# Kernel optimization log

Measured on AMD Instinct MI355X. Metric: run time of the kernel, lower is better.

The kernel has to match this reference:

```python
import jax, jax.numpy as jnp
import numpy as np

PI = float(np.pi)          # ouro.pi_center
THIRD = 2.0 * PI / 3.0     # ouro.third_offset
EPB = PI                   # ouro.effective_pi_boundary
DEV = 0.01                 # ouro.deviation
SPARSITY = 0.75
NH = 8
EPS = 1e-5


def prune(w):
    # ouroboros_prune_revive: elementwise resonance chain + quantile threshold mask
    s = w.size
    bloom = jnp.clip(jnp.sin(w * PI), -1.0, 1.0)  # noise_level = 0 (deterministic)
    theta = jnp.linspace(0.0, float(s), s).reshape(w.shape)
    bloom = bloom + bloom * jnp.cos(theta / float(s) + THIRD) * 1.5  # rebound_amp
    etched = jnp.cos(bloom * (EPB ** 2)) + bloom * bloom * (DEV / PI)
    thr = jnp.quantile(jnp.abs(etched), 1.0 - SPARSITY)
    mask = (jnp.abs(etched) > thr).astype(w.dtype)
    return w * mask


def layernorm(x, g, b):
    m = jnp.mean(x, axis=-1, keepdims=True)
    v = jnp.var(x, axis=-1, keepdims=True)
    return (x - m) * jax.lax.rsqrt(v + EPS) * g + b


def setup_inputs():
    key = jax.random.key(0)
    V, D, L, F, B, S = 10000, 512, 6, 2048, 16, 512
    ks = jax.random.split(key, 9)
    p = lambda k, sh: jax.random.normal(k, sh, jnp.float32) * 0.02
    return dict(
        src=jax.random.randint(ks[0], (B, S), 0, V),
        emb=p(ks[1], (V, D)),
        pos=p(ks[2], (1, 512, D)),
        in_proj_w=p(ks[3], (L, 3 * D, D)), in_proj_b=jnp.zeros((L, 3 * D), jnp.float32),
        out_proj_w=p(ks[4], (L, D, D)), out_proj_b=jnp.zeros((L, D), jnp.float32),
        ln1_g=jnp.ones((L, D), jnp.float32), ln1_b=jnp.zeros((L, D), jnp.float32),
        ln2_g=jnp.ones((L, D), jnp.float32), ln2_b=jnp.zeros((L, D), jnp.float32),
        lin1_w=p(ks[5], (L, F, D)), lin1_b=jnp.zeros((L, F), jnp.float32),
        lin2_w=p(ks[6], (L, D, F)), lin2_b=jnp.zeros((L, D), jnp.float32),
        out_w=p(ks[7], (V, D)), out_b=jnp.zeros((V,), jnp.float32),
    )


def reference(src, emb, pos, in_proj_w, in_proj_b, out_proj_w, out_proj_b,
              ln1_g, ln1_b, ln2_g, ln2_b, lin1_w, lin1_b, lin2_w, lin2_b,
              out_w, out_b):
    B, S = src.shape
    D = emb.shape[1]
    L = in_proj_w.shape[0]
    H, dh = NH, D // NH
    x = emb[src] * jnp.sqrt(jnp.float32(D)) + pos[:, :S, :]
    for l in range(L):
        wi = prune(in_proj_w[l])
        qkv = x @ wi.T + in_proj_b[l]
        q, k, v = jnp.split(qkv, 3, axis=-1)
        q = q.reshape(B, S, H, dh)
        k = k.reshape(B, S, H, dh)
        v = v.reshape(B, S, H, dh)
        scores = jnp.einsum('bqhd,bkhd->bhqk', q, k) / jnp.sqrt(jnp.float32(dh))
        att = jax.nn.softmax(scores, axis=-1)
        o = jnp.einsum('bhqk,bkhd->bqhd', att, v).reshape(B, S, D)
        o = o @ out_proj_w[l].T + out_proj_b[l]
        x = layernorm(x + o, ln1_g[l], ln1_b[l])  # post-norm
        w1 = prune(lin1_w[l])
        w2 = prune(lin2_w[l])
        ff = jax.nn.relu(x @ w1.T + lin1_b[l]) @ w2.T + lin2_b[l]
        x = layernorm(x + ff, ln2_g[l], ln2_b[l])
    return x @ out_w.T + out_b
```

## Files before the change

kernel.cpp:

```cpp
#include <hip/hip_runtime.h>
#include <math.h>

#define MTOK   8192
#define DMODEL 512
#define DFF    2048
#define NLAYER 6
#define VOCAB  10000
#define VPAD   10112
#define NHEAD  8
#define DHEAD  64

typedef __attribute__((ext_vector_type(8))) __bf16 bf16x8;
typedef __attribute__((ext_vector_type(4))) float  f32x4;

static const size_t X_B     = 0;
static const size_t Y_B     = (size_t)MTOK * DMODEL * 4;
static const size_t SH_B    = Y_B * 2;
static const size_t WH_B    = SH_B + (size_t)MTOK * DFF * 4;
static const size_t WL_B    = WH_B + (size_t)DFF * DMODEL * 2;
static const size_t HIST_B  = WL_B + (size_t)DFF * DMODEL * 2;
static const size_t STATE_B = HIST_B + (size_t)36 * 4096 * 4;
static const size_t THR_B   = STATE_B + (size_t)36 * 32;
static const size_t WS_BASE = THR_B + 18 * 8;
static const size_t BITS_B  = (WS_BASE + 255) & ~(size_t)255;
static const size_t WS_BITS = BITS_B + (size_t)17301504 / 8;

struct PState {
    double lo, hi;
    unsigned int rank;
    unsigned int pad;
    unsigned long long found;
};

__device__ __forceinline__ unsigned short f2b(float f)
{
    unsigned int u = __float_as_uint(f);
    u += 0x7fffu + ((u >> 16) & 1u);
    return (unsigned short)(u >> 16);
}
__device__ __forceinline__ float b2f(unsigned short h)
{
    return __uint_as_float(((unsigned int)h) << 16);
}

__device__ __forceinline__ void gload16(const void* g, void* l)
{
    __builtin_amdgcn_global_load_lds(
        (const __attribute__((address_space(1))) unsigned int*)g,
        (__attribute__((address_space(3))) unsigned int*)l, 16, 0, 0);
}

__device__ __forceinline__ double etched_abs(float wv, int i, double step, double invn)
{
    float b0 = sinf(wv * 3.14159274f);
    b0 = fminf(1.0f, fmaxf(-1.0f, b0));
    double theta = step * (double)i;
    double c = cos(theta * invn + 2.0943951023931953);
    double bl = (double)b0;
    double bloom = bl + bl * c * 1.5;
    double e = cos(bloom * 9.869604401089358)
             + bloom * bloom * 0.003183098861837907;
    return fabs(e);
}

__device__ __forceinline__ void prune_matrix(int m, const float* ipw, const float* w1,
                                             const float* w2, const float** w, int* n)
{
    int l = m / 3, j = m % 3;
    if (j == 0)      { *w = ipw + (size_t)l * 786432;  *n = 786432;  }
    else if (j == 1) { *w = w1  + (size_t)l * 1048576; *n = 1048576; }
    else             { *w = w2  + (size_t)l * 1048576; *n = 1048576; }
}

__device__ __forceinline__ size_t moff9(int j)
{
    int c0 = (j + 2) / 3;
    return (size_t)c0 * 786432 + (size_t)(j - c0) * 1048576;
}
static __host__ __device__ inline size_t prune_soff(int m)
{
    int c0 = (m + 2) / 3;
    return (size_t)c0 * 786432 + (size_t)(m - c0) * 1048576;
}

__global__ __launch_bounds__(256) void k_prune_init(unsigned int* hist, PState* st)
{
    int gid = blockIdx.x * 256 + threadIdx.x;
    for (int i = gid; i < 36 * 4096; i += gridDim.x * 256) hist[i] = 0u;
    if (gid < 36) {
        int m = gid >> 1;
        int n = (m % 3 == 0) ? 786432 : 1048576;
        st[gid].lo = 0.0;
        st[gid].hi = 1.03;
        st[gid].rank = (unsigned)(n / 4 - 1 + (gid & 1));
        st[gid].found = 0x7FF0000000000000ULL;
    }
}

__global__ __launch_bounds__(256) void k_eval(const float* ipw, const float* w1,
                                              const float* w2, double* E, int mb0)
{
    int j = blockIdx.x >> 7;
    int chunk = blockIdx.x & 127;
    int m = mb0 + j;
    const float* w; int n;
    prune_matrix(m, ipw, w1, w2, &w, &n);
    double* Em = E + moff9(j);
    double step = (double)n / (double)(n - 1);
    double invn = 1.0 / (double)n;
    int per = (n + 127) >> 7;
    int i0 = chunk * per;
    int i1 = min(n, i0 + per);
    for (int i = i0 + (int)threadIdx.x; i < i1; i += 256)
        Em[i] = etched_abs(w[i], i, step, invn);
}

__global__ __launch_bounds__(256) void k_hist_E(const double* __restrict__ E,
                                                unsigned int* hist, PState* st, int mb0)
{
    int j = blockIdx.x >> 6;
    int chunk = blockIdx.x & 63;
    int m = mb0 + j;
    int n = (m % 3 == 0) ? 786432 : 1048576;
    const double* Em = E + moff9(j);
    __shared__ unsigned int h[2][4096];
    for (int i = threadIdx.x; i < 8192; i += 256) ((unsigned int*)h)[i] = 0u;
    __syncthreads();
    double lo0 = st[2*m].lo,   hi0 = st[2*m].hi;
    double lo1 = st[2*m+1].lo, hi1 = st[2*m+1].hi;
    double sc0 = 4096.0 / (hi0 - lo0);
    double sc1 = 4096.0 / (hi1 - lo1);
    int per = (n + 63) >> 6;
    int i0 = chunk * per;
    int i1 = min(n, i0 + per);
    for (int i = i0 + (int)threadIdx.x; i < i1; i += 256) {
        double a = Em[i];
        if (a >= lo0 && a < hi0) {
            int bin = (int)((a - lo0) * sc0); if (bin > 4095) bin = 4095;
            atomicAdd(&h[0][bin], 1u);
        }
        if (a >= lo1 && a < hi1) {
            int bin = (int)((a - lo1) * sc1); if (bin > 4095) bin = 4095;
            atomicAdd(&h[1][bin], 1u);
        }
    }
    __syncthreads();
    for (int i = threadIdx.x; i < 4096; i += 256) {
        if (h[0][i]) atomicAdd(&hist[(size_t)(2*m) * 4096 + i], h[0][i]);
        if (h[1][i]) atomicAdd(&hist[(size_t)(2*m+1) * 4096 + i], h[1][i]);
    }
}

__global__ __launch_bounds__(256) void k_prune_select(unsigned int* hist, PState* st,
                                                      int mb0)
{
    int s = mb0 * 2 + blockIdx.x;
    __shared__ unsigned int h[4096];
    unsigned int* gh = hist + (size_t)s * 4096;
    for (int i = threadIdx.x; i < 4096; i += 256) { h[i] = gh[i]; gh[i] = 0u; }
    __syncthreads();
    if (threadIdx.x == 0) {
        PState ps = st[s];
        unsigned int r = ps.rank;
        unsigned int acc = 0;
        int bsel = -1; unsigned int newr = 0;
        for (int bi = 0; bi < 4096; ++bi) {
            unsigned int c = h[bi];
            if (bsel < 0 && r < acc + c) { bsel = bi; newr = r - acc; }
            acc += c;
        }
        if (bsel < 0) {
            for (int bi = 4095; bi >= 0; --bi)
                if (h[bi]) { bsel = bi; newr = h[bi] - 1; break; }
            if (bsel < 0) { bsel = 0; newr = 0; }
        }
        double width = (ps.hi - ps.lo) / 4096.0;
        st[s].lo = ps.lo + width * bsel;
        st[s].hi = ps.lo + width * (bsel + 1);
        st[s].rank = newr;
    }
}

__global__ __launch_bounds__(256) void k_capture_E(const double* __restrict__ E,
                                                   PState* st, int mb0)
{
    int j = blockIdx.x >> 6;
    int chunk = blockIdx.x & 63;
    int m = mb0 + j;
    int n = (m % 3 == 0) ? 786432 : 1048576;
    const double* Em = E + moff9(j);
    double lo0 = st[2*m].lo, lo1 = st[2*m+1].lo;
    unsigned long long mn0 = 0x7FF0000000000000ULL, mn1 = 0x7FF0000000000000ULL;
    int per = (n + 63) >> 6;
    int i0 = chunk * per;
    int i1 = min(n, i0 + per);
    for (int i = i0 + (int)threadIdx.x; i < i1; i += 256) {
        double a = Em[i];
        unsigned long long bits = (unsigned long long)__double_as_longlong(a);
        if (a >= lo0 && bits < mn0) mn0 = bits;
        if (a >= lo1 && bits < mn1) mn1 = bits;
    }
    __shared__ unsigned long long sm[2];
    if (threadIdx.x == 0) { sm[0] = 0x7FF0000000000000ULL; sm[1] = 0x7FF0000000000000ULL; }
    __syncthreads();
    atomicMin(&sm[0], mn0);
    atomicMin(&sm[1], mn1);
    __syncthreads();
    if (threadIdx.x == 0) {
        atomicMin(&st[2*m].found, sm[0]);
        atomicMin(&st[2*m+1].found, sm[1]);
    }
}

__global__ void k_thr_batch(PState* st, double* thr, int mb0)
{
    int t = threadIdx.x;
    if (t < 9) {
        int m = mb0 + t;
        double v0 = __longlong_as_double((long long)st[2*m].found);
        double v1 = __longlong_as_double((long long)st[2*m+1].found);
        thr[m] = v0 + 0.75 * (v1 - v0);
    }
}

__global__ __launch_bounds__(256) void k_bits(const double* __restrict__ E,
                                              const double* __restrict__ thr,
                                              unsigned long long* __restrict__ bits,
                                              int mb0)
{
    int j = blockIdx.y;
    int m = mb0 + j;
    int n = (m % 3 == 0) ? 786432 : 1048576;
    double T = thr[m];
    const double* Em = E + moff9(j);
    unsigned long long* bm = bits + (prune_soff(m) >> 6);
    int nw = n >> 6;
    int lane = threadIdx.x & 63;
    int wid = (blockIdx.x * 256 + threadIdx.x) >> 6;
    int nwaves = gridDim.x * 4;
    for (int w = wid; w < nw; w += nwaves) {
        bool p = Em[(w << 6) + lane] > T;
        unsigned long long b = __ballot(p);
        if (lane == 0) bm[w] = b;
    }
}

__global__ __launch_bounds__(256) void k_mask_bits(const float* __restrict__ w,
                                                   unsigned short* __restrict__ oh,
                                                   unsigned short* __restrict__ ol,
                                                   const unsigned long long* __restrict__ bits,
                                                   int n)
{
    int stride = gridDim.x * 256 * 4;
    for (int i4 = (blockIdx.x * 256 + threadIdx.x) * 4; i4 < n; i4 += stride) {
        float4 v = *(const float4*)(w + i4);
        unsigned long long word = bits[i4 >> 6];
        int sh = i4 & 63;
        float x0 = (word >> (sh + 0)) & 1 ? v.x : 0.0f;
        float x1 = (word >> (sh + 1)) & 1 ? v.y : 0.0f;
        float x2 = (word >> (sh + 2)) & 1 ? v.z : 0.0f;
        float x3 = (word >> (sh + 3)) & 1 ? v.w : 0.0f;
        unsigned short h0 = f2b(x0), h1 = f2b(x1), h2 = f2b(x2), h3 = f2b(x3);
        uint2 hv, lv;
        hv.x = (unsigned)h0 | ((unsigned)h1 << 16);
        hv.y = (unsigned)h2 | ((unsigned)h3 << 16);
        lv.x = (unsigned)f2b(x0 - b2f(h0)) | ((unsigned)f2b(x1 - b2f(h1)) << 16);
        lv.y = (unsigned)f2b(x2 - b2f(h2)) | ((unsigned)f2b(x3 - b2f(h3)) << 16);
        *(uint2*)(oh + i4) = hv;
        *(uint2*)(ol + i4) = lv;
    }
}

__global__ __launch_bounds__(256) void k_apply_mask_split(const float* __restrict__ w,
                                                          unsigned short* __restrict__ oh,
                                                          unsigned short* __restrict__ ol,
                                                          const double* __restrict__ thr,
                                                          int m, int n)
{
    double T = thr[m];
    double step = (double)n / (double)(n - 1);
    double invn = 1.0 / (double)n;
    for (int i = blockIdx.x * 256 + threadIdx.x; i < n; i += gridDim.x * 256) {
        double a = etched_abs(w[i], i, step, invn);
        float v = (a > T) ? w[i] : 0.0f;
        unsigned short h = f2b(v);
        oh[i] = h;
        ol[i] = f2b(v - b2f(h));
    }
}

__global__ __launch_bounds__(256) void k_split(const float* __restrict__ w,
                                               unsigned short* __restrict__ oh,
                                               unsigned short* __restrict__ ol,
                                               int n, int total)
{
    for (int i = blockIdx.x * 256 + threadIdx.x; i < total; i += gridDim.x * 256) {
        float v = (i < n) ? w[i] : 0.0f;
        unsigned short h = f2b(v);
        oh[i] = h;
        ol[i] = f2b(v - b2f(h));
    }
}

__global__ __launch_bounds__(256) void k_embed(const int* __restrict__ src,
                                               const float* __restrict__ emb,
                                               const float* __restrict__ pos,
                                               float* __restrict__ x,
                                               unsigned short* __restrict__ xh,
                                               unsigned short* __restrict__ xl)
{
    int t = blockIdx.x;
    int tid = threadIdx.x;
    int v = src[t];
    int s = t & 511;
    const float* e = emb + (size_t)v * DMODEL;
    const float* p = pos + (size_t)s * DMODEL;
    size_t base = (size_t)t * DMODEL;
    float y0 = e[tid]       * 22.627416997969522f + p[tid];
    float y1 = e[tid + 256] * 22.627416997969522f + p[tid + 256];
    x[base + tid] = y0;
    x[base + tid + 256] = y1;
    unsigned short h0 = f2b(y0), h1 = f2b(y1);
    xh[base + tid] = h0;        xl[base + tid] = f2b(y0 - b2f(h0));
    xh[base + tid + 256] = h1;  xl[base + tid + 256] = f2b(y1 - b2f(h1));
}

__global__ __launch_bounds__(256) void k_gemm_mfma(const unsigned short* __restrict__ AH,
                                                   const unsigned short* __restrict__ AL,
                                                   const unsigned short* __restrict__ BH,
                                                   const unsigned short* __restrict__ BL,
                                                   const float* __restrict__ bias,
                                                   float* __restrict__ C,
                                                   unsigned short* __restrict__ CH,
                                                   unsigned short* __restrict__ CL,
                                                   int M, int N, int K, int mode)
{
    __shared__ __align__(16) unsigned char LA[16384];
    __shared__ __align__(16) unsigned char LB[16384];
    unsigned char* LAH = LA;
    unsigned char* LAL = LA + 8192;
    unsigned char* LBH = LB;
    unsigned char* LBL = LB + 8192;

    const int t    = threadIdx.x;
    const int lane = t & 63;
    const int wv   = t >> 6;
    const int wm   = wv >> 1;
    const int wn   = wv & 1;
    const int rowBase = blockIdx.y * 128;
    const int colBase = blockIdx.x * 128;

    const f32x4 zero = {0.0f, 0.0f, 0.0f, 0.0f};
    f32x4 acc[4][4];
#pragma unroll
    for (int i = 0; i < 4; ++i)
#pragma unroll
        for (int j = 0; j < 4; ++j) acc[i][j] = zero;

    int aoff[4], boff[4];
#pragma unroll
    for (int i = 0; i < 4; ++i) {
        int ra = (wm << 6) + (i << 4) + (lane & 15);
        aoff[i] = ra * 64 + (((lane >> 4) ^ ((ra >> 1) & 3)) << 4);
        int rb = (wn << 6) + (i << 4) + (lane & 15);
        boff[i] = rb * 64 + (((lane >> 4) ^ ((rb >> 1) & 3)) << 4);
    }

    int o0 = (wv << 10) + (lane << 4);
    int r0s = o0 >> 6;
    int k0s = (((o0 >> 4) & 3) ^ ((r0s >> 1) & 3)) << 3;
    int o1 = o0 + 4096;
    int r1s = o1 >> 6;
    int k1s = (((o1 >> 4) & 3) ^ ((r1s >> 1) & 3)) << 3;
    int ldsb0 = (wv << 10);
    int ldsb1 = (wv << 10) + 4096;

    for (int k0 = 0; k0 < K; k0 += 32) {
        __syncthreads();
        size_t ga0 = (size_t)(rowBase + r0s) * K + (k0 + k0s);
        size_t ga1 = (size_t)(rowBase + r1s) * K + (k0 + k1s);
        size_t gb0 = (size_t)(colBase + r0s) * K + (k0 + k0s);
        size_t gb1 = (size_t)(colBase + r1s) * K + (k0 + k1s);
        gload16(AH + ga0, LAH + ldsb0);
        gload16(AL + ga0, LAL + ldsb0);
        gload16(BH + gb0, LBH + ldsb0);
        gload16(BL + gb0, LBL + ldsb0);
        gload16(AH + ga1, LAH + ldsb1);
        gload16(AL + ga1, LAL + ldsb1);
        gload16(BH + gb1, LBH + ldsb1);
        gload16(BL + gb1, LBL + ldsb1);
        __syncthreads();

        bf16x8 ah[4], alo[4], bh[4], blo[4];
#pragma unroll
        for (int i = 0; i < 4; ++i) {
            ah[i]  = *(const bf16x8*)(LAH + aoff[i]);
            alo[i] = *(const bf16x8*)(LAL + aoff[i]);
            bh[i]  = *(const bf16x8*)(LBH + boff[i]);
            blo[i] = *(const bf16x8*)(LBL + boff[i]);
        }
#pragma unroll
        for (int i = 0; i < 4; ++i)
#pragma unroll
            for (int j = 0; j < 4; ++j) {
                acc[i][j] = __builtin_amdgcn_mfma_f32_16x16x32_bf16(alo[i], bh[j],  acc[i][j], 0, 0, 0);
                acc[i][j] = __builtin_amdgcn_mfma_f32_16x16x32_bf16(ah[i],  blo[j], acc[i][j], 0, 0, 0);
                acc[i][j] = __builtin_amdgcn_mfma_f32_16x16x32_bf16(ah[i],  bh[j],  acc[i][j], 0, 0, 0);
            }
    }

#pragma unroll
    for (int j = 0; j < 4; ++j) {
        int col = colBase + (wn << 6) + (j << 4) + (lane & 15);
        if (col < N) {
            float bv = bias[col];
#pragma unroll
            for (int i = 0; i < 4; ++i) {
                int row0 = rowBase + (wm << 6) + (i << 4) + ((lane >> 4) << 2);
#pragma unroll
                for (int r = 0; r < 4; ++r) {
                    float v = acc[i][j][r] + bv;
                    size_t idx = (size_t)(row0 + r) * N + col;
                    if (mode) {
                        v = fmaxf(v, 0.0f);
                        unsigned short hh = f2b(v);
                        CH[idx] = hh;
                        CL[idx] = f2b(v - b2f(hh));
                    } else {
                        C[idx] = v;
                    }
                }
            }
        }
    }
}

__global__ __launch_bounds__(256) void k_attn(const float* __restrict__ qkv,
                                              unsigned short* __restrict__ oh,
                                              unsigned short* __restrict__ ol)
{
    __shared__ float Qs[64][68];
    __shared__ float KP[64][68];
    __shared__ float Vs[64][64];
    __shared__ float red[64][17];
    __shared__ float mS[64], lS[64], aS[64];

    int bh = blockIdx.x;
    int b = bh >> 3, h = bh & 7;
    int qt = blockIdx.y;
    int t = threadIdx.x;
    int tx = t & 15, ty = t >> 4;
    int r0 = ty * 4, c0 = tx * 4;
    int rowq = b * 512 + qt * 64;

    size_t baseq = (size_t)rowq * 1536 + h * 64;
#pragma unroll
    for (int u = 0; u < 4; ++u) {
        int f = t + u * 256;
        int r = f >> 4;
        int d4 = (f & 15) << 2;
        float4 q4 = *(const float4*)(qkv + baseq + (size_t)r * 1536 + d4);
        Qs[d4 + 0][r] = q4.x; Qs[d4 + 1][r] = q4.y;
        Qs[d4 + 2][r] = q4.z; Qs[d4 + 3][r] = q4.w;
    }
    float O[4][4];
#pragma unroll
    for (int i = 0; i < 4; ++i)
#pragma unroll
        for (int j = 0; j < 4; ++j) O[i][j] = 0.0f;
    if (t < 64) { mS[t] = -INFINITY; lS[t] = 0.0f; }

    size_t basek = (size_t)(b * 512) * 1536 + h * 64;
    for (int kt = 0; kt < 8; ++kt) {
        __syncthreads();
#pragma unroll
        for (int u = 0; u < 4; ++u) {
            int f = t + u * 256;
            int r = f >> 4;
            int d4 = (f & 15) << 2;
            size_t g = basek + (size_t)(kt * 64 + r) * 1536 + d4;
            float4 k4 = *(const float4*)(qkv + g + 512);
            KP[d4 + 0][r] = k4.x; KP[d4 + 1][r] = k4.y;
            KP[d4 + 2][r] = k4.z; KP[d4 + 3][r] = k4.w;
            float4 v4 = *(const float4*)(qkv + g + 1024);
            *(float4*)&Vs[r][d4] = v4;
        }
        __syncthreads();
        float S[4][4];
#pragma unroll
        for (int i = 0; i < 4; ++i)
#pragma unroll
            for (int j = 0; j < 4; ++j) S[i][j] = 0.0f;
#pragma unroll 16
        for (int d = 0; d < 64; ++d) {
            float4 qa = *(const float4*)&Qs[d][r0];
            float4 kb = *(const float4*)&KP[d][c0];
            const float* qa_ = &qa.x;
            const float* kb_ = &kb.x;
#pragma unroll
            for (int i = 0; i < 4; ++i)
#pragma unroll
                for (int j = 0; j < 4; ++j)
                    S[i][j] = fmaf(qa_[i], kb_[j], S[i][j]);
        }
#pragma unroll
        for (int i = 0; i < 4; ++i) {
            float mx = fmaxf(fmaxf(S[i][0], S[i][1]), fmaxf(S[i][2], S[i][3]));
            red[r0 + i][tx] = mx * 0.125f;
        }
        __syncthreads();
        if (t < 64) {
            float m = red[t][0];
#pragma unroll
            for (int k = 1; k < 16; ++k) m = fmaxf(m, red[t][k]);
            float mo = mS[t];
            float mn = fmaxf(mo, m);
            aS[t] = __expf(mo - mn);
            mS[t] = mn;
        }
        __syncthreads();
#pragma unroll
        for (int i = 0; i < 4; ++i) {
            float mn = mS[r0 + i];
            float rs = 0.0f;
#pragma unroll
            for (int j = 0; j < 4; ++j) {
                float p = __expf(fmaf(S[i][j], 0.125f, -mn));
                S[i][j] = p;
                rs += p;
            }
            red[r0 + i][tx] = rs;
            *(float4*)&KP[r0 + i][c0] = *(float4*)S[i];
        }
        __syncthreads();
        if (t < 64) {
            float s = red[t][0];
#pragma unroll
            for (int k = 1; k < 16; ++k) s += red[t][k];
            lS[t] = lS[t] * aS[t] + s;
        }
        float pv[4][4];
#pragma unroll
        for (int i = 0; i < 4; ++i)
#pragma unroll
            for (int j = 0; j < 4; ++j) pv[i][j] = 0.0f;
#pragma unroll 4
        for (int c4 = 0; c4 < 64; c4 += 4) {
            float pr[4][4];
#pragma unroll
            for (int i = 0; i < 4; ++i)
                *(float4*)pr[i] = *(const float4*)&KP[r0 + i][c4];
#pragma unroll
            for (int cc = 0; cc < 4; ++cc) {
                float4 v = *(const float4*)&Vs[c4 + cc][c0];
                const float* v_ = &v.x;
#pragma unroll
                for (int i = 0; i < 4; ++i)
#pragma unroll
                    for (int j = 0; j < 4; ++j)
                        pv[i][j] = fmaf(pr[i][cc], v_[j], pv[i][j]);
            }
        }
#pragma unroll
        for (int i = 0; i < 4; ++i) {
            float a = aS[r0 + i];
#pragma unroll
            for (int j = 0; j < 4; ++j) O[i][j] = O[i][j] * a + pv[i][j];
        }
    }
    __syncthreads();
#pragma unroll
    for (int i = 0; i < 4; ++i) {
        float inv = 1.0f / lS[r0 + i];
        float o0 = O[i][0] * inv, o1 = O[i][1] * inv;
        float o2 = O[i][2] * inv, o3 = O[i][3] * inv;
        size_t idx = (size_t)(rowq + r0 + i) * 512 + h * 64 + c0;
        unsigned short h0 = f2b(o0), h1 = f2b(o1), h2 = f2b(o2), h3 = f2b(o3);
        uint2 hv, lv;
        hv.x = (unsigned)h0 | ((unsigned)h1 << 16);
        hv.y = (unsigned)h2 | ((unsigned)h3 << 16);
        lv.x = (unsigned)f2b(o0 - b2f(h0)) | ((unsigned)f2b(o1 - b2f(h1)) << 16);
        lv.y = (unsigned)f2b(o2 - b2f(h2)) | ((unsigned)f2b(o3 - b2f(h3)) << 16);
        *(uint2*)(oh + idx) = hv;
        *(uint2*)(ol + idx) = lv;
    }
}

__global__ __launch_bounds__(256) void k_ln(const float* x, const float* r,
                                            const float* __restrict__ g,
                                            const float* __restrict__ b,
                                            float* out,
                                            unsigned short* __restrict__ outh,
                                            unsigned short* __restrict__ outl)
{
    int t = blockIdx.x, tid = threadIdx.x;
    size_t base = (size_t)t * DMODEL;
    float a0 = x[base + tid]       + r[base + tid];
    float a1 = x[base + tid + 256] + r[base + tid + 256];
    float s = a0 + a1;
    float q = fmaf(a0, a0, a1 * a1);
#pragma unroll
    for (int off = 32; off; off >>= 1) {
        s += __shfl_xor(s, off, 64);
        q += __shfl_xor(q, off, 64);
    }
    __shared__ float sw[8];
    int w = tid >> 6, lane = tid & 63;
    if (lane == 0) { sw[w] = s; sw[4 + w] = q; }
    __syncthreads();
    s = sw[0] + sw[1] + sw[2] + sw[3];
    q = sw[4] + sw[5] + sw[6] + sw[7];
    float mean = s * (1.0f / 512.0f);
    float var = q * (1.0f / 512.0f) - mean * mean;
    float inv = 1.0f / sqrtf(var + 1e-5f);
    float y0 = (a0 - mean) * inv * g[tid]       + b[tid];
    float y1 = (a1 - mean) * inv * g[tid + 256] + b[tid + 256];
    out[base + tid]       = y0;
    out[base + tid + 256] = y1;
    unsigned short h0 = f2b(y0), h1 = f2b(y1);
    outh[base + tid] = h0;        outl[base + tid] = f2b(y0 - b2f(h0));
    outh[base + tid + 256] = h1;  outl[base + tid + 256] = f2b(y1 - b2f(h1));
}

static inline void launch_gemm_f32(const unsigned short* AH, const unsigned short* AL,
                                   const unsigned short* BH, const unsigned short* BL,
                                   const float* bias, float* C, int M, int N, int K,
                                   hipStream_t stream)
{
    dim3 grid((N + 127) / 128, M / 128);
    k_gemm_mfma<<<grid, 256, 0, stream>>>(AH, AL, BH, BL, bias, C, nullptr, nullptr,
                                          M, N, K, 0);
}
static inline void launch_gemm_split(const unsigned short* AH, const unsigned short* AL,
                                     const unsigned short* BH, const unsigned short* BL,
                                     const float* bias, unsigned short* CH,
                                     unsigned short* CL, int M, int N, int K,
                                     hipStream_t stream)
{
    dim3 grid((N + 127) / 128, M / 128);
    k_gemm_mfma<<<grid, 256, 0, stream>>>(AH, AL, BH, BL, bias, nullptr, CH, CL,
                                          M, N, K, 1);
}

extern "C" void kernel_launch(void* const* d_in, const int* in_sizes, int n_in,
                              void* d_out, int out_size, void* d_ws, size_t ws_size,
                              hipStream_t stream)
{
    (void)in_sizes; (void)n_in; (void)out_size;
    if (ws_size < WS_BASE) return;
    const bool use_bits = (ws_size >= WS_BITS);

    const int*   src = (const int*)  d_in[0];
    const float* emb = (const float*)d_in[1];
    const float* pos = (const float*)d_in[2];
    const float* ipw = (const float*)d_in[3];
    const float* ipb = (const float*)d_in[4];
    const float* opw = (const float*)d_in[5];
    const float* opb = (const float*)d_in[6];
    const float* ln1g = (const float*)d_in[7];
    const float* ln1b = (const float*)d_in[8];
    const float* ln2g = (const float*)d_in[9];
    const float* ln2b = (const float*)d_in[10];
    const float* w1  = (const float*)d_in[11];
    const float* bb1 = (const float*)d_in[12];
    const float* w2  = (const float*)d_in[13];
    const float* bb2 = (const float*)d_in[14];
    const float* ow  = (const float*)d_in[15];
    const float* ob  = (const float*)d_in[16];

    char* ws = (char*)d_ws;
    float* X   = (float*)(ws + X_B);
    float* Yf  = (float*)(ws + Y_B);
    float* SHf = (float*)(ws + SH_B);
    double* E  = (double*)(ws + X_B);
    unsigned short* YS_H = (unsigned short*)(ws + Y_B);
    unsigned short* YS_L = (unsigned short*)(ws + Y_B + 8388608);
    unsigned short* XS_H = (unsigned short*)(ws + SH_B + 50331648);
    unsigned short* XS_L = (unsigned short*)(ws + SH_B + 58720256);
    unsigned short* FH   = (unsigned short*)(ws + SH_B);
    unsigned short* FL   = (unsigned short*)(ws + SH_B + 33554432);
    unsigned short* OWH  = (unsigned short*)(ws + SH_B);
    unsigned short* OWL  = (unsigned short*)(ws + SH_B + (size_t)VPAD * DMODEL * 2);
    unsigned short* WH = (unsigned short*)(ws + WH_B);
    unsigned short* WL = (unsigned short*)(ws + WL_B);
    unsigned int* HIST = (unsigned int*)(ws + HIST_B);
    PState* ST = (PState*)(ws + STATE_B);
    double* THR = (double*)(ws + THR_B);
    unsigned long long* BITS = (unsigned long long*)(ws + BITS_B);
    float* OUT = (float*)d_out;

    k_prune_init<<<64, 256, 0, stream>>>(HIST, ST);
    for (int b = 0; b < 2; ++b) {
        int mb0 = b * 9;
        k_eval<<<9 * 128, 256, 0, stream>>>(ipw, w1, w2, E, mb0);
        for (int lev = 0; lev < 3; ++lev) {
            k_hist_E<<<9 * 64, 256, 0, stream>>>(E, HIST, ST, mb0);
            k_prune_select<<<18, 256, 0, stream>>>(HIST, ST, mb0);
        }
        k_capture_E<<<9 * 64, 256, 0, stream>>>(E, ST, mb0);
        k_thr_batch<<<1, 32, 0, stream>>>(ST, THR, mb0);
        if (use_bits)
            k_bits<<<dim3(64, 9), 256, 0, stream>>>(E, THR, BITS, mb0);
    }

    k_embed<<<MTOK, 256, 0, stream>>>(src, emb, pos, X, XS_H, XS_L);

    for (int l = 0; l < NLAYER; ++l) {
        if (use_bits)
            k_mask_bits<<<256, 256, 0, stream>>>(ipw + (size_t)l * 786432, WH, WL,
                                                 BITS + (prune_soff(3 * l) >> 6), 786432);
        else
            k_apply_mask_split<<<1024, 256, 0, stream>>>(ipw + (size_t)l * 786432, WH, WL,
                                                         THR, 3 * l, 786432);
        launch_gemm_f32(XS_H, XS_L, WH, WL, ipb + (size_t)l * 1536, SHf,
                        MTOK, 1536, DMODEL, stream);
        k_attn<<<dim3(128, 8), 256, 0, stream>>>(SHf, YS_H, YS_L);
        k_split<<<512, 256, 0, stream>>>(opw + (size_t)l * 262144, WH, WL, 262144, 262144);
        launch_gemm_f32(YS_H, YS_L, WH, WL, opb + (size_t)l * 512, SHf,
                        MTOK, DMODEL, DMODEL, stream);
        k_ln<<<MTOK, 256, 0, stream>>>(X, SHf, ln1g + (size_t)l * 512,
                                       ln1b + (size_t)l * 512, X, YS_H, YS_L);
        if (use_bits)
            k_mask_bits<<<256, 256, 0, stream>>>(w1 + (size_t)l * 1048576, WH, WL,
                                                 BITS + (prune_soff(3 * l + 1) >> 6), 1048576);
        else
            k_apply_mask_split<<<1024, 256, 0, stream>>>(w1 + (size_t)l * 1048576, WH, WL,
                                                         THR, 3 * l + 1, 1048576);
        launch_gemm_split(YS_H, YS_L, WH, WL, bb1 + (size_t)l * 2048, FH, FL,
                          MTOK, DFF, DMODEL, stream);
        if (use_bits)
            k_mask_bits<<<256, 256, 0, stream>>>(w2 + (size_t)l * 1048576, WH, WL,
                                                 BITS + (prune_soff(3 * l + 2) >> 6), 1048576);
        else
            k_apply_mask_split<<<1024, 256, 0, stream>>>(w2 + (size_t)l * 1048576, WH, WL,
                                                         THR, 3 * l + 2, 1048576);
        launch_gemm_f32(FH, FL, WH, WL, bb2 + (size_t)l * 512, Yf,
                        MTOK, DMODEL, DFF, stream);
        k_ln<<<MTOK, 256, 0, stream>>>(X, Yf, ln2g + (size_t)l * 512,
                                       ln2b + (size_t)l * 512, X, XS_H, XS_L);
    }

    k_split<<<2048, 256, 0, stream>>>(ow, OWH, OWL, VOCAB * DMODEL, VPAD * DMODEL);
    launch_gemm_f32(XS_H, XS_L, OWH, OWL, ob, OUT, MTOK, VOCAB, DMODEL, stream);
}
```

Baseline: 4.869 ms.

## Select prune thresholds with float32 histograms and double-precision band refinement

Replaces the materialized double-precision etched array with on-the-fly float32 evaluation in the histogram and capture passes. Exact double values are recomputed only for candidates inside a narrow band around the float-estimated quantile, and a per-matrix refine kernel selects the exact threshold from them. Mask application also uses the float32 fast path and falls back to double only near the threshold. It further adds XCD-aware workgroup remapping in the GEMM. This aims to cut the double-precision transcendental cost and the E-array memory traffic, at the cost of correctness depending on BAND and CCAP being large enough.

```diff
diff --git a/kernel.cpp b/kernel.cpp
--- a/kernel.cpp
+++ b/kernel.cpp
@@ -10,6 +10,9 @@
 #define NHEAD  8
 #define DHEAD  64
 
+#define BAND   1.0e-3f
+#define CCAP   131072
+
 typedef __attribute__((ext_vector_type(8))) __bf16 bf16x8;
 typedef __attribute__((ext_vector_type(4))) float  f32x4;
 
@@ -21,9 +24,9 @@
 static const size_t HIST_B  = WL_B + (size_t)DFF * DMODEL * 2;
 static const size_t STATE_B = HIST_B + (size_t)36 * 4096 * 4;
 static const size_t THR_B   = STATE_B + (size_t)36 * 32;
-static const size_t WS_BASE = THR_B + 18 * 8;
-static const size_t BITS_B  = (WS_BASE + 255) & ~(size_t)255;
-static const size_t WS_BITS = BITS_B + (size_t)17301504 / 8;
+static const size_t WS_NEED = THR_B + 18 * 8;
+static const size_t CVAL_B  = 0;
+static const size_t CMETA_B = (size_t)18 * CCAP * 8;
 
 struct PState {
     double lo, hi;
@@ -63,6 +66,16 @@
     return fabs(e);
 }
 
+__device__ __forceinline__ float etched_abs32(float wv, int i, float inv_nm1)
+{
+    float b0 = sinf(wv * 3.14159274f);
+    b0 = fminf(1.0f, fmaxf(-1.0f, b0));
+    float c = __cosf(fmaf((float)i, inv_nm1, 2.0943951f));
+    float bloom = fmaf(b0 * 1.5f, c, b0);
+    float e = fmaf(bloom * bloom, 0.0031830989f, __cosf(bloom * 9.8696044f));
+    return fabsf(e);
+}
+
 __device__ __forceinline__ void prune_matrix(int m, const float* ipw, const float* w1,
                                              const float* w2, const float** w, int* n)
 {
@@ -72,22 +85,13 @@
     else             { *w = w2  + (size_t)l * 1048576; *n = 1048576; }
 }
 
-__device__ __forceinline__ size_t moff9(int j)
-{
-    int c0 = (j + 2) / 3;
-    return (size_t)c0 * 786432 + (size_t)(j - c0) * 1048576;
-}
-static __host__ __device__ inline size_t prune_soff(int m)
-{
-    int c0 = (m + 2) / 3;
-    return (size_t)c0 * 786432 + (size_t)(m - c0) * 1048576;
-}
-
-__global__ __launch_bounds__(256) void k_prune_init(unsigned int* hist, PState* st)
+__global__ __launch_bounds__(256) void k_prune_init(unsigned int* hist, PState* st,
+                                                    unsigned int* meta)
 {
     int gid = blockIdx.x * 256 + threadIdx.x;
     for (int i = gid; i < 36 * 4096; i += gridDim.x * 256) hist[i] = 0u;
     if (gid < 36) {
+        meta[gid] = 0u;
         int m = gid >> 1;
         int n = (m % 3 == 0) ? 786432 : 1048576;
         st[gid].lo = 0.0;
@@ -97,32 +101,15 @@
     }
 }
 
-__global__ __launch_bounds__(256) void k_eval(const float* ipw, const float* w1,
-                                              const float* w2, double* E, int mb0)
-{
-    int j = blockIdx.x >> 7;
-    int chunk = blockIdx.x & 127;
-    int m = mb0 + j;
+__global__ __launch_bounds__(256) void k_hist32(const float* ipw, const float* w1,
+                                                const float* w2,
+                                                unsigned int* hist, PState* st)
+{
+    int m = blockIdx.y;
+    int chunk = blockIdx.x;
     const float* w; int n;
     prune_matrix(m, ipw, w1, w2, &w, &n);
-    double* Em = E + moff9(j);
-    double step = (double)n / (double)(n - 1);
-    double invn = 1.0 / (double)n;
-    int per = (n + 127) >> 7;
-    int i0 = chunk * per;
-    int i1 = min(n, i0 + per);
-    for (int i = i0 + (int)threadIdx.x; i < i1; i += 256)
-        Em[i] = etched_abs(w[i], i, step, invn);
-}
-
-__global__ __launch_bounds__(256) void k_hist_E(const double* __restrict__ E,
-                                                unsigned int* hist, PState* st, int mb0)
-{
-    int j = blockIdx.x >> 6;
-    int chunk = blockIdx.x & 63;
-    int m = mb0 + j;
-    int n = (m % 3 == 0) ? 786432 : 1048576;
-    const double* Em = E + moff9(j);
+    float inv_nm1 = 1.0f / (float)(n - 1);
     __shared__ unsigned int h[2][4096];
     for (int i = threadIdx.x; i < 8192; i += 256) ((unsigned int*)h)[i] = 0u;
     __syncthreads();
@@ -134,7 +121,7 @@
     int i0 = chunk * per;
     int i1 = min(n, i0 + per);
     for (int i = i0 + (int)threadIdx.x; i < i1; i += 256) {
-        double a = Em[i];
+        double a = (double)etched_abs32(w[i], i, inv_nm1);
         if (a >= lo0 && a < hi0) {
             int bin = (int)((a - lo0) * sc0); if (bin > 4095) bin = 4095;
             atomicAdd(&h[0][bin], 1u);
@@ -151,10 +138,9 @@
     }
 }
 
-__global__ __launch_bounds__(256) void k_prune_select(unsigned int* hist, PState* st,
-                                                      int mb0)
-{
-    int s = mb0 * 2 + blockIdx.x;
+__global__ __launch_bounds__(256) void k_prune_select(unsigned int* hist, PState* st)
+{
+    int s = blockIdx.x;
     __shared__ unsigned int h[4096];
     unsigned int* gh = hist + (size_t)s * 4096;
     for (int i = threadIdx.x; i < 4096; i += 256) { h[i] = gh[i]; gh[i] = 0u; }
@@ -181,22 +167,23 @@
     }
 }
 
-__global__ __launch_bounds__(256) void k_capture_E(const double* __restrict__ E,
-                                                   PState* st, int mb0)
-{
-    int j = blockIdx.x >> 6;
-    int chunk = blockIdx.x & 63;
-    int m = mb0 + j;
-    int n = (m % 3 == 0) ? 786432 : 1048576;
-    const double* Em = E + moff9(j);
+__global__ __launch_bounds__(256) void k_capture32(const float* ipw, const float* w1,
+                                                   const float* w2, PState* st)
+{
+    int m = blockIdx.y;
+    int chunk = blockIdx.x;
+    const float* w; int n;
+    prune_matrix(m, ipw, w1, w2, &w, &n);
+    float inv_nm1 = 1.0f / (float)(n - 1);
     double lo0 = st[2*m].lo, lo1 = st[2*m+1].lo;
     unsigned long long mn0 = 0x7FF0000000000000ULL, mn1 = 0x7FF0000000000000ULL;
     int per = (n + 63) >> 6;
     int i0 = chunk * per;
     int i1 = min(n, i0 + per);
     for (int i = i0 + (int)threadIdx.x; i < i1; i += 256) {
-        double a = Em[i];
-        unsigned long long bits = (unsigned long long)__double_as_longlong(a);
+        float e = etched_abs32(w[i], i, inv_nm1);
+        double a = (double)e;
+        unsigned long long bits = (unsigned long long)__float_as_uint(e);
         if (a >= lo0 && bits < mn0) mn0 = bits;
         if (a >= lo1 && bits < mn1) mn1 = bits;
     }
@@ -212,77 +199,138 @@
     }
 }
 
-__global__ void k_thr_batch(PState* st, double* thr, int mb0)
-{
-    int t = threadIdx.x;
-    if (t < 9) {
-        int m = mb0 + t;
-        double v0 = __longlong_as_double((long long)st[2*m].found);
-        double v1 = __longlong_as_double((long long)st[2*m+1].found);
-        thr[m] = v0 + 0.75 * (v1 - v0);
-    }
-}
-
-__global__ __launch_bounds__(256) void k_bits(const double* __restrict__ E,
-                                              const double* __restrict__ thr,
-                                              unsigned long long* __restrict__ bits,
-                                              int mb0)
-{
-    int j = blockIdx.y;
-    int m = mb0 + j;
+__global__ __launch_bounds__(256) void k_collect(const float* ipw, const float* w1,
+                                                 const float* w2, const PState* st,
+                                                 unsigned int* meta, double* cval)
+{
+    int m = blockIdx.y;
+    int chunk = blockIdx.x;
+    const float* w; int n;
+    prune_matrix(m, ipw, w1, w2, &w, &n);
+    float inv_nm1 = 1.0f / (float)(n - 1);
+    float vA = __uint_as_float((unsigned int)st[2*m].found);
+    float vB = __uint_as_float((unsigned int)st[2*m+1].found);
+    float bandLo = vA - BAND;
+    float bandHi = vB + BAND;
+    double* cv = cval + (size_t)m * CCAP;
+    double step = (double)n / (double)(n - 1);
+    double invn = 1.0 / (double)n;
+    unsigned int loc = 0;
+    int per = (n + 63) >> 6;
+    int i0 = chunk * per;
+    int i1 = min(n, i0 + per);
+    for (int i = i0 + (int)threadIdx.x; i < i1; i += 256) {
+        float e = etched_abs32(w[i], i, inv_nm1);
+        if (e < bandLo) ++loc;
+        else if (e <= bandHi) {
+            unsigned int s = atomicAdd(&meta[m], 1u);
+            if (s < CCAP) cv[s] = etched_abs(w[i], i, step, invn);
+        }
+    }
+    __shared__ unsigned int sred[256];
+    sred[threadIdx.x] = loc;
+    __syncthreads();
+    for (int s = 128; s; s >>= 1) {
+        if (threadIdx.x < (unsigned)s) sred[threadIdx.x] += sred[threadIdx.x + s];
+        __syncthreads();
+    }
+    if (threadIdx.x == 0) atomicAdd(&meta[18 + m], sred[0]);
+}
+
+__global__ __launch_bounds__(256) void k_refine(const PState* st,
+                                                const unsigned int* meta,
+                                                const double* cval, double* thr)
+{
+    int m = blockIdx.x;
+    int tid = threadIdx.x;
     int n = (m % 3 == 0) ? 786432 : 1048576;
-    double T = thr[m];
-    const double* Em = E + moff9(j);
-    unsigned long long* bm = bits + (prune_soff(m) >> 6);
-    int nw = n >> 6;
-    int lane = threadIdx.x & 63;
-    int wid = (blockIdx.x * 256 + threadIdx.x) >> 6;
-    int nwaves = gridDim.x * 4;
-    for (int w = wid; w < nw; w += nwaves) {
-        bool p = Em[(w << 6) + lane] > T;
-        unsigned long long b = __ballot(p);
-        if (lane == 0) bm[w] = b;
-    }
-}
-
-__global__ __launch_bounds__(256) void k_mask_bits(const float* __restrict__ w,
+    unsigned int C = meta[m]; if (C > CCAP) C = CCAP;
+    unsigned int B = meta[18 + m];
+    const double* cv = cval + (size_t)m * CCAP;
+    float vA = __uint_as_float((unsigned int)st[2*m].found);
+    float vB = __uint_as_float((unsigned int)st[2*m+1].found);
+    double lo = (double)vA - 2.0 * (double)BAND;
+    double hi = (double)vB + 2.0 * (double)BAND;
+    double sc = 4096.0 / (hi - lo);
+
+    __shared__ unsigned int h[4096];
+    __shared__ double buf[4096];
+    __shared__ int nbuf;
+    __shared__ int bsel;
+    __shared__ unsigned int accb;
+    __shared__ double tsel[2];
+    for (int i = tid; i < 4096; i += 256) h[i] = 0u;
+    __syncthreads();
+    for (unsigned int i = tid; i < C; i += 256) {
+        int b = (int)((cv[i] - lo) * sc);
+        b = max(0, min(4095, b));
+        atomicAdd(&h[b], 1u);
+    }
+    __syncthreads();
+
+    long k0 = (long)(n / 4 - 1);
+    for (int t = 0; t < 2; ++t) {
+        long r = k0 + t - (long)B;
+        if (r < 0) r = 0;
+        if (r >= (long)C) r = (long)C - 1;
+        if (tid == 0) {
+            unsigned int acc = 0; int bs = 4095; unsigned int ab = 0;
+            for (int b = 0; b < 4096; ++b) {
+                unsigned int c = h[b];
+                if ((unsigned long)r < acc + c) { bs = b; ab = acc; break; }
+                acc += c;
+            }
+            bsel = bs; accb = ab; nbuf = 0;
+            tsel[t] = (double)vA;
+        }
+        __syncthreads();
+        for (unsigned int i = tid; i < C; i += 256) {
+            int b = (int)((cv[i] - lo) * sc);
+            b = max(0, min(4095, b));
+            if (b == bsel) {
+                int s = atomicAdd(&nbuf, 1);
+                if (s < 4096) buf[s] = cv[i];
+            }
+        }
+        __syncthreads();
+        int len = min(nbuf, 4096);
+        long rin = r - (long)accb;
+        if (rin < 0) rin = 0;
+        if (rin >= len) rin = len - 1;
+        for (int i = tid; i < len; i += 256) {
+            double v = buf[i];
+            long rk = 0;
+            for (int j = 0; j < len; ++j) {
+                double u = buf[j];
+                if (u < v || (u == v && j < i)) ++rk;
+            }
+            if (rk == rin) tsel[t] = v;
+        }
+        __syncthreads();
+    }
+    if (tid == 0) thr[m] = tsel[0] + 0.75 * (tsel[1] - tsel[0]);
+}
+
+__global__ __launch_bounds__(256) void k_mask_fast(const float* __restrict__ w,
                                                    unsigned short* __restrict__ oh,
                                                    unsigned short* __restrict__ ol,
-                                                   const unsigned long long* __restrict__ bits,
-                                                   int n)
-{
-    int stride = gridDim.x * 256 * 4;
-    for (int i4 = (blockIdx.x * 256 + threadIdx.x) * 4; i4 < n; i4 += stride) {
-        float4 v = *(const float4*)(w + i4);
-        unsigned long long word = bits[i4 >> 6];
-        int sh = i4 & 63;
-        float x0 = (word >> (sh + 0)) & 1 ? v.x : 0.0f;
-        float x1 = (word >> (sh + 1)) & 1 ? v.y : 0.0f;
-        float x2 = (word >> (sh + 2)) & 1 ? v.z : 0.0f;
-        float x3 = (word >> (sh + 3)) & 1 ? v.w : 0.0f;
-        unsigned short h0 = f2b(x0), h1 = f2b(x1), h2 = f2b(x2), h3 = f2b(x3);
-        uint2 hv, lv;
-        hv.x = (unsigned)h0 | ((unsigned)h1 << 16);
-        hv.y = (unsigned)h2 | ((unsigned)h3 << 16);
-        lv.x = (unsigned)f2b(x0 - b2f(h0)) | ((unsigned)f2b(x1 - b2f(h1)) << 16);
-        lv.y = (unsigned)f2b(x2 - b2f(h2)) | ((unsigned)f2b(x3 - b2f(h3)) << 16);
-        *(uint2*)(oh + i4) = hv;
-        *(uint2*)(ol + i4) = lv;
-    }
-}
-
-__global__ __launch_bounds__(256) void k_apply_mask_split(const float* __restrict__ w,
-                                                          unsigned short* __restrict__ oh,
-                                                          unsigned short* __restrict__ ol,
-                                                          const double* __restrict__ thr,
-                                                          int m, int n)
+                                                   const double* __restrict__ thr,
+                                                   int m, int n)
 {
     double T = thr[m];
+    double tLo = T - (double)BAND;
+    double tHi = T + (double)BAND;
+    float inv_nm1 = 1.0f / (float)(n - 1);
     double step = (double)n / (double)(n - 1);
     double invn = 1.0 / (double)n;
     for (int i = blockIdx.x * 256 + threadIdx.x; i < n; i += gridDim.x * 256) {
-        double a = etched_abs(w[i], i, step, invn);
-        float v = (a > T) ? w[i] : 0.0f;
+        float wv = w[i];
+        double a = (double)etched_abs32(wv, i, inv_nm1);
+        bool keep;
+        if (a > tHi) keep = true;
+        else if (a < tLo) keep = false;
+        else keep = etched_abs(wv, i, step, invn) > T;
+        float v = keep ? wv : 0.0f;
         unsigned short h = f2b(v);
         oh[i] = h;
         ol[i] = f2b(v - b2f(h));
@@ -347,8 +395,16 @@
     const int wv   = t >> 6;
     const int wm   = wv >> 1;
     const int wn   = wv & 1;
-    const int rowBase = blockIdx.y * 128;
-    const int colBase = blockIdx.x * 128;
+
+    int gx = gridDim.x;
+    int wg = blockIdx.y * gx + blockIdx.x;
+    int nwg = gx * gridDim.y;
+    {
+        int q = nwg >> 3, r = nwg & 7, xcd = wg & 7, ord = wg >> 3;
+        wg = (xcd < r ? xcd * (q + 1) : r * (q + 1) + (xcd - r) * q) + ord;
+    }
+    const int rowBase = (wg / gx) * 128;
+    const int colBase = (wg % gx) * 128;
 
     const f32x4 zero = {0.0f, 0.0f, 0.0f, 0.0f};
     f32x4 acc[4][4];
@@ -647,8 +703,7 @@
                               hipStream_t stream)
 {
     (void)in_sizes; (void)n_in; (void)out_size;
-    if (ws_size < WS_BASE) return;
-    const bool use_bits = (ws_size >= WS_BITS);
+    if (ws_size < WS_NEED) return;
 
     const int*   src = (const int*)  d_in[0];
     const float* emb = (const float*)d_in[1];
@@ -672,7 +727,8 @@
     float* X   = (float*)(ws + X_B);
     float* Yf  = (float*)(ws + Y_B);
     float* SHf = (float*)(ws + SH_B);
-    double* E  = (double*)(ws + X_B);
+    double* CVAL = (double*)(ws + CVAL_B);
+    unsigned int* META = (unsigned int*)(ws + CMETA_B);
     unsigned short* YS_H = (unsigned short*)(ws + Y_B);
     unsigned short* YS_L = (unsigned short*)(ws + Y_B + 8388608);
     unsigned short* XS_H = (unsigned short*)(ws + SH_B + 50331648);
@@ -686,32 +742,22 @@
     unsigned int* HIST = (unsigned int*)(ws + HIST_B);
     PState* ST = (PState*)(ws + STATE_B);
     double* THR = (double*)(ws + THR_B);
-    unsigned long long* BITS = (unsigned long long*)(ws + BITS_B);
     float* OUT = (float*)d_out;
 
-    k_prune_init<<<64, 256, 0, stream>>>(HIST, ST);
-    for (int b = 0; b < 2; ++b) {
-        int mb0 = b * 9;
-        k_eval<<<9 * 128, 256, 0, stream>>>(ipw, w1, w2, E, mb0);
-        for (int lev = 0; lev < 3; ++lev) {
-            k_hist_E<<<9 * 64, 256, 0, stream>>>(E, HIST, ST, mb0);
-            k_prune_select<<<18, 256, 0, stream>>>(HIST, ST, mb0);
-        }
-        k_capture_E<<<9 * 64, 256, 0, stream>>>(E, ST, mb0);
-        k_thr_batch<<<1, 32, 0, stream>>>(ST, THR, mb0);
-        if (use_bits)
-            k_bits<<<dim3(64, 9), 256, 0, stream>>>(E, THR, BITS, mb0);
-    }
+    k_prune_init<<<64, 256, 0, stream>>>(HIST, ST, META);
+    for (int lev = 0; lev < 3; ++lev) {
+        k_hist32<<<dim3(64, 18), 256, 0, stream>>>(ipw, w1, w2, HIST, ST);
+        k_prune_select<<<36, 256, 0, stream>>>(HIST, ST);
+    }
+    k_capture32<<<dim3(64, 18), 256, 0, stream>>>(ipw, w1, w2, ST);
+    k_collect<<<dim3(64, 18), 256, 0, stream>>>(ipw, w1, w2, ST, META, CVAL);
+    k_refine<<<18, 256, 0, stream>>>(ST, META, CVAL, THR);
 
     k_embed<<<MTOK, 256, 0, stream>>>(src, emb, pos, X, XS_H, XS_L);
 
     for (int l = 0; l < NLAYER; ++l) {
-        if (use_bits)
-            k_mask_bits<<<256, 256, 0, stream>>>(ipw + (size_t)l * 786432, WH, WL,
-                                                 BITS + (prune_soff(3 * l) >> 6), 786432);
-        else
-            k_apply_mask_split<<<1024, 256, 0, stream>>>(ipw + (size_t)l * 786432, WH, WL,
-                                                         THR, 3 * l, 786432);
+        k_mask_fast<<<512, 256, 0, stream>>>(ipw + (size_t)l * 786432, WH, WL,
+                                             THR, 3 * l, 786432);
         launch_gemm_f32(XS_H, XS_L, WH, WL, ipb + (size_t)l * 1536, SHf,
                         MTOK, 1536, DMODEL, stream);
         k_attn<<<dim3(128, 8), 256, 0, stream>>>(SHf, YS_H, YS_L);
@@ -720,20 +766,12 @@
                         MTOK, DMODEL, DMODEL, stream);
         k_ln<<<MTOK, 256, 0, stream>>>(X, SHf, ln1g + (size_t)l * 512,
                                        ln1b + (size_t)l * 512, X, YS_H, YS_L);
-        if (use_bits)
-            k_mask_bits<<<256, 256, 0, stream>>>(w1 + (size_t)l * 1048576, WH, WL,
-                                                 BITS + (prune_soff(3 * l + 1) >> 6), 1048576);
-        else
-            k_apply_mask_split<<<1024, 256, 0, stream>>>(w1 + (size_t)l * 1048576, WH, WL,
-                                                         THR, 3 * l + 1, 1048576);
+        k_mask_fast<<<512, 256, 0, stream>>>(w1 + (size_t)l * 1048576, WH, WL,
+                                             THR, 3 * l + 1, 1048576);
         launch_gemm_split(YS_H, YS_L, WH, WL, bb1 + (size_t)l * 2048, FH, FL,
                           MTOK, DFF, DMODEL, stream);
-        if (use_bits)
-            k_mask_bits<<<256, 256, 0, stream>>>(w2 + (size_t)l * 1048576, WH, WL,
-                                                 BITS + (prune_soff(3 * l + 2) >> 6), 1048576);
-        else
-            k_apply_mask_split<<<1024, 256, 0, stream>>>(w2 + (size_t)l * 1048576, WH, WL,
-                                                         THR, 3 * l + 2, 1048576);
+        k_mask_fast<<<512, 256, 0, stream>>>(w2 + (size_t)l * 1048576, WH, WL,
+                                             THR, 3 * l + 2, 1048576);
         launch_gemm_f32(FH, FL, WH, WL, bb2 + (size_t)l * 512, Yf,
                         MTOK, DMODEL, DFF, stream);
         k_ln<<<MTOK, 256, 0, stream>>>(X, Yf, ln2g + (size_t)l * 512,
```

Measured after the change: 6.176 ms. 1.27x slower.
